# Optimization experiments

Measured on AMD Instinct MI355X. Metric: run time of the kernel, lower is better.

The kernel has to match this reference:

```python
import jax, jax.numpy as jnp
import numpy as np

N = 100   # num_nodes
D = 32    # num_dags
B = 8192  # batch_size
H = 32    # MLP hidden width


def setup_inputs() -> dict:
    key = jax.random.key(0)
    ks = jax.random.split(key, 6)
    x = jax.random.normal(ks[0], (B, N), dtype=jnp.float32)
    # binary adjacency masks for each sampled DAG
    A = (jax.random.uniform(ks[1], (D, N, N)) < 0.5).astype(jnp.float32)
    # per-dag topological order: a permutation of the N nodes
    order = jax.vmap(lambda k: jax.random.permutation(k, N))(
        jax.random.split(ks[2], D)).astype(jnp.int32)
    do_idx = 0  # intervened node
    # per-node MLP params: Linear(N+1, H) -> LeakyReLU -> Linear(H, 1)
    W1 = jax.random.normal(ks[3], (N, H, N + 1), dtype=jnp.float32) * (1.0 / np.sqrt(N + 1))
    b1 = jnp.zeros((N, H), dtype=jnp.float32)
    W2 = jax.random.normal(ks[4], (N, H), dtype=jnp.float32) * (1.0 / np.sqrt(H))
    b2 = jnp.zeros((N,), dtype=jnp.float32)
    return {"x": x, "A": A, "order": order, "do_idx": do_idx,
            "W1": W1, "b1": b1, "W2": W2, "b2": b2}


def reference(x, A, order, do_idx, W1, b1, W2, b2):
    Bn, Nn = x.shape
    # intervention: zero incoming edges of do_idx
    A = A.at[:, :, do_idx].set(0.0)

    def run_dag(A_d, order_d):
        def step(outputs, node):
            mask = A_d[:, node]                      # [N] parents of `node`
            ins = jnp.concatenate(
                [outputs * mask[None, :], x[:, node][:, None]], axis=1)  # [B, N+1]
            h = jax.nn.leaky_relu(ins @ W1[node].T + b1[node])           # [B, H]
            out = h @ W2[node] + b2[node]                                # [B]
            val = jnp.where(node == do_idx, x[:, node], out)
            return outputs.at[:, node].set(val), None

        outs, _ = jax.lax.scan(step, jnp.zeros((Bn, Nn), x.dtype), order_d)
        return outs  # [B, N]

    return jax.vmap(run_dag)(A, order)  # [D, B, N]
```

## Files before the change

kernel.cpp:

```cpp
#include <hip/hip_runtime.h>
#include <hip/hip_fp16.h>

#define NN 100
#define HH 32
#define BB 8192
#define DD 32
#define KP 128
#define TPB 512

typedef _Float16 f16x8 __attribute__((ext_vector_type(8)));
typedef _Float16 f16x2 __attribute__((ext_vector_type(2)));
typedef __fp16 fph2 __attribute__((ext_vector_type(2)));
typedef float f32x4 __attribute__((ext_vector_type(4)));
typedef unsigned short ushort_t;
typedef unsigned int uint_t;
union FU { uint4 u; f16x8 h; };
union PU { fph2 p; f16x2 h; uint_t u; };

#define AS_GLOBAL __attribute__((address_space(1)))
#define AS_LDS    __attribute__((address_space(3)))

__global__ void prep_xth(const float* __restrict__ x, ushort_t* __restrict__ xTh) {
  int idx = blockIdx.x * 256 + threadIdx.x;
  if (idx >= BB * NN) return;
  int b = idx & (BB - 1);
  int n = idx >> 13;
  xTh[idx] = __half_as_ushort(__float2half_rn(x[(size_t)b * NN + n]));
}

__global__ void prep_w1m(const float* __restrict__ A, const float* __restrict__ W1,
                         const float* __restrict__ b1, ushort_t* __restrict__ W1M) {
  int idx = blockIdx.x * 256 + threadIdx.x;
  int tile = idx >> 12;
  int d = tile / NN;
  int node = tile - d * NN;
  int rem = idx & 4095;
  int j = rem >> 7;
  int k = rem & 127;
  float v = 0.f;
  if (k < NN) {
    float m = A[((size_t)d * NN + k) * NN + node];
    v = (m != 0.f) ? W1[((size_t)node * HH + j) * (NN + 1) + k] : 0.f;
  } else if (k == NN) {
    v = W1[((size_t)node * HH + j) * (NN + 1) + NN];
  } else if (k == NN + 1) {
    v = b1[node * HH + j];
  }
  int t = (j * KP + k) ^ ((j & 7) << 3);
  W1M[(size_t)tile * 4096 + t] = __half_as_ushort(__float2half_rn(v));
}

__global__ void prep_epi3(const float* __restrict__ W2, const float* __restrict__ b2,
                          uint_t* __restrict__ epi) {
  int idx = blockIdx.x * 256 + threadIdx.x;
  if (idx >= NN * 20) return;
  int node = idx / 20;
  int c = idx - node * 20;
  uint_t v = 0u;
  if (c < 16) {
    uint_t lo = __half_as_ushort(__float2half_rn(W2[node * HH + 2 * c]));
    uint_t hi = __half_as_ushort(__float2half_rn(W2[node * HH + 2 * c + 1]));
    v = lo | (hi << 16);
  } else if (c == 16) {
    v = __float_as_uint(b2[node]);
  }
  epi[idx] = v;
}

#define XS_OFF 65536
#define EPI_OFF 73728
#define SMEM_BYTES (73728 + 8000)

__global__ __launch_bounds__(TPB, 4) void dag_mfma_ss(
    const ushort_t* __restrict__ xTh,
    const int* __restrict__ order,
    const int* __restrict__ do_idx_p,
    const ushort_t* __restrict__ W1M,
    const uint_t* __restrict__ epi_g,
    float* __restrict__ out)
{
  __shared__ __align__(16) char smem[SMEM_BYTES];
  ushort_t* stage = (ushort_t*)smem;
  const char* sp = (const char*)smem;
  uint_t* epi_l = (uint_t*)(smem + EPI_OFF);

  const int d = blockIdx.y;
  const int bx = blockIdx.x;
  const int tid = threadIdx.x;
  const int w = tid >> 6;
  const int lane = tid & 63;
  const int g = lane >> 4;
  const int n16 = lane & 15;
  const int di = __builtin_amdgcn_readfirstlane(do_idx_p[0]);

  {
    const uint4* s4 = (const uint4*)epi_g;
    uint4* d4 = (uint4*)epi_l;
    for (int i = tid; i < 500; i += TPB) d4[i] = s4[i];
  }

  const ushort_t* Wd = W1M + (size_t)d * NN * 4096;
  const int* ord = order + d * NN;

  int vs[4];
#pragma unroll
  for (int S = 0; S < 4; ++S) {
    int hw = n16 * 128 + ((8 * g) ^ ((n16 & 3) << 3)) + 32 * (S ^ ((n16 >> 2) & 1));
    vs[S] = 2 * hw + 32768;
  }
  int xso = XS_OFF + (w * 64 + n16) * 2 + 4096;

  int nd[4], nn[4];
#pragma unroll
  for (int q = 0; q < 4; ++q) nd[q] = __builtin_amdgcn_readfirstlane(ord[q]);
#pragma unroll
  for (int q = 0; q < 4; ++q) {
    const ushort_t* gsrc = Wd + (size_t)nd[q] * 4096 + tid * 8;
    __builtin_amdgcn_global_load_lds((const AS_GLOBAL void*)gsrc,
        (AS_LDS void*)(stage + q * 4096 + (w << 9)), 16, 0, 0);
  }
#pragma unroll
  for (int q = 0; q < 4; ++q) {
    if (w == q) {
      const ushort_t* gx = xTh + (size_t)nd[q] * BB + bx * 512 + lane * 8;
      __builtin_amdgcn_global_load_lds((const AS_GLOBAL void*)gx,
          (AS_LDS void*)(smem + XS_OFF + q * 1024), 16, 0, 0);
    }
  }

  uint4 breg[4][4];
#pragma unroll
  for (int nt = 0; nt < 4; ++nt) {
#pragma unroll
    for (int S = 0; S < 4; ++S) breg[nt][S] = make_uint4(0u, 0u, 0u, 0u);
    breg[nt][3].z = (g == 0) ? 0x3C000000u : 0u;
  }

  const f32x4 zero4 = {0.f, 0.f, 0.f, 0.f};
  PU c001; c001.u = 0x211F211Fu;

#pragma unroll 1
  for (int ss = 0; ss < 25; ++ss) {
    asm volatile("s_waitcnt vmcnt(0) lgkmcnt(0)" ::: "memory");
    __builtin_amdgcn_s_barrier();
    __builtin_amdgcn_sched_barrier(0);

#pragma unroll
    for (int S = 0; S < 4; ++S) vs[S] ^= 32768;
    xso ^= 4096;

    const bool more = (ss < 24);
    if (more) {
#pragma unroll
      for (int q = 0; q < 4; ++q)
        nn[q] = __builtin_amdgcn_readfirstlane(ord[4 * (ss + 1) + q]);
      const int dsts = (((ss + 1) & 1) << 14);
#pragma unroll
      for (int q = 0; q < 4; ++q) {
        const ushort_t* gsrc = Wd + (size_t)nn[q] * 4096 + tid * 8;
        __builtin_amdgcn_global_load_lds((const AS_GLOBAL void*)gsrc,
            (AS_LDS void*)(stage + dsts + q * 4096 + (w << 9)), 16, 0, 0);
      }
      const int xdst = XS_OFF + (((ss + 1) & 1) << 12);
#pragma unroll
      for (int q = 0; q < 4; ++q) {
        if (w == q) {
          const ushort_t* gx = xTh + (size_t)nn[q] * BB + bx * 512 + lane * 8;
          __builtin_amdgcn_global_load_lds((const AS_GLOBAL void*)gx,
              (AS_LDS void*)(smem + xdst + q * 1024), 16, 0, 0);
        }
      }
    }

#pragma unroll
    for (int q = 0; q < 4; ++q) {
      const int node = nd[q];

      ushort_t xb[4];
#pragma unroll
      for (int nt = 0; nt < 4; ++nt)
        xb[nt] = *(const ushort_t*)(sp + xso + q * 1024 + nt * 32);

#pragma unroll
      for (int nt = 0; nt < 4; ++nt) {
        uint_t ins = 0x3C000000u | (uint_t)xb[nt];
        breg[nt][3].z = (g == 0) ? ins : breg[nt][3].z;
      }

      float val[4];
      if (node != di) {
        const char* ep = (const char*)epi_l + node * 80;
        const float b2n = *(const float*)(ep + 64);

        f32x4 acc[4];
        float p0[4];

        {
          __builtin_amdgcn_s_setprio(1);
#pragma unroll
          for (int S = 0; S < 4; ++S) {
            FU a0;
            a0.u = *(const uint4*)(sp + vs[S] + q * 8192);
#pragma unroll
            for (int nt = 0; nt < 4; ++nt) {
              FU bu; bu.u = breg[nt][S];
              if (S == 0)
                acc[nt] = __builtin_amdgcn_mfma_f32_16x16x32_f16(a0.h, bu.h, zero4, 0, 0, 0);
              else
                acc[nt] = __builtin_amdgcn_mfma_f32_16x16x32_f16(a0.h, bu.h, acc[nt], 0, 0, 0);
            }
          }
          __builtin_amdgcn_s_setprio(0);
          const uint2 wlo = *(const uint2*)(ep + 8 * g);
          PU w01, w23; w01.u = wlo.x; w23.u = wlo.y;
#pragma unroll
          for (int nt = 0; nt < 4; ++nt) {
            PU h01, h23;
            h01.p = __builtin_amdgcn_cvt_pkrtz(acc[nt][0], acc[nt][1]);
            h23.p = __builtin_amdgcn_cvt_pkrtz(acc[nt][2], acc[nt][3]);
            h01.p = __builtin_elementwise_max(h01.p, h01.p * c001.p);
            h23.p = __builtin_elementwise_max(h23.p, h23.p * c001.p);
            float p = __builtin_amdgcn_fdot2(h01.h, w01.h, 0.f, false);
            p0[nt] = __builtin_amdgcn_fdot2(h23.h, w23.h, p, false);
          }
        }

        {
          __builtin_amdgcn_s_setprio(1);
#pragma unroll
          for (int S = 0; S < 4; ++S) {
            FU a1;
            a1.u = *(const uint4*)(sp + vs[S] + q * 8192 + 4096);
#pragma unroll
            for (int nt = 0; nt < 4; ++nt) {
              FU bu; bu.u = breg[nt][S];
              if (S == 0)
                acc[nt] = __builtin_amdgcn_mfma_f32_16x16x32_f16(a1.h, bu.h, zero4, 0, 0, 0);
              else
                acc[nt] = __builtin_amdgcn_mfma_f32_16x16x32_f16(a1.h, bu.h, acc[nt], 0, 0, 0);
            }
          }
          __builtin_amdgcn_s_setprio(0);
          const uint2 whi = *(const uint2*)(ep + 32 + 8 * g);
          PU w45, w67; w45.u = whi.x; w67.u = whi.y;
#pragma unroll
          for (int nt = 0; nt < 4; ++nt) {
            PU h45, h67;
            h45.p = __builtin_amdgcn_cvt_pkrtz(acc[nt][0], acc[nt][1]);
            h67.p = __builtin_amdgcn_cvt_pkrtz(acc[nt][2], acc[nt][3]);
            h45.p = __builtin_elementwise_max(h45.p, h45.p * c001.p);
            h67.p = __builtin_elementwise_max(h67.p, h67.p * c001.p);
            float p = __builtin_amdgcn_fdot2(h45.h, w45.h, p0[nt], false);
            p = __builtin_amdgcn_fdot2(h67.h, w67.h, p, false);
            p += __shfl_xor(p, 16, 64);
            p += __shfl_xor(p, 32, 64);
            val[nt] = p + b2n;
          }
        }
      } else {
#pragma unroll
        for (int nt = 0; nt < 4; ++nt)
          val[nt] = __half2float(__ushort_as_half(xb[nt]));
      }

      const int sn = node >> 5;
      const int en2 = (node >> 1) & 3;
      const int gn = (node >> 3) & 3;
      const int hin = node & 1;
      const bool own = (g == gn);
      ushort_t hv[4];
#pragma unroll
      for (int nt = 0; nt < 4; ++nt) hv[nt] = __half_as_ushort(__float2half_rn(val[nt]));
#pragma unroll
      for (int S = 0; S < 4; ++S) {
        if (S != sn) continue;
#pragma unroll
        for (int nt = 0; nt < 4; ++nt) {
          uint4& Bq = breg[nt][S];
          uint_t hvn = (uint_t)hv[nt];
          if (en2 == 0) {
            uint_t old = Bq.x;
            uint_t nw = hin ? ((old & 0x0000FFFFu) | (hvn << 16)) : ((old & 0xFFFF0000u) | hvn);
            Bq.x = own ? nw : old;
          } else if (en2 == 1) {
            uint_t old = Bq.y;
            uint_t nw = hin ? ((old & 0x0000FFFFu) | (hvn << 16)) : ((old & 0xFFFF0000u) | hvn);
            Bq.y = own ? nw : old;
          } else if (en2 == 2) {
            uint_t old = Bq.z;
            uint_t nw = hin ? ((old & 0x0000FFFFu) | (hvn << 16)) : ((old & 0xFFFF0000u) | hvn);
            Bq.z = own ? nw : old;
          } else {
            uint_t old = Bq.w;
            uint_t nw = hin ? ((old & 0x0000FFFFu) | (hvn << 16)) : ((old & 0xFFFF0000u) | hvn);
            Bq.w = own ? nw : old;
          }
        }
      }
    }

#pragma unroll
    for (int q = 0; q < 4; ++q) nd[q] = nn[q];
  }

  ushort_t* tbuf = (ushort_t*)smem;
  for (int c = 0; c < 8; ++c) {
    __syncthreads();
    if (w == c) {
#pragma unroll
      for (int nt = 0; nt < 4; ++nt) {
        int r = nt * 16 + n16;
#pragma unroll
        for (int S = 0; S < 4; ++S) {
          int k = 32 * S + 8 * g;
          *(uint2*)&tbuf[r * 132 + k] = make_uint2(breg[nt][S].x, breg[nt][S].y);
          *(uint2*)&tbuf[r * 132 + k + 4] = make_uint2(breg[nt][S].z, breg[nt][S].w);
        }
      }
    }
    __syncthreads();
    const size_t obase = ((size_t)d * BB + bx * 512 + c * 64) * NN;
    for (int idx = tid; idx < 64 * NN; idx += TPB) {
      int rl = idx / NN;
      int col = idx - rl * NN;
      out[obase + idx] = __half2float(__ushort_as_half(tbuf[rl * 132 + col]));
    }
  }
}

extern "C" void kernel_launch(void* const* d_in, const int* in_sizes, int n_in,
                              void* d_out, int out_size, void* d_ws, size_t ws_size,
                              hipStream_t stream) {
  const float* x     = (const float*)d_in[0];
  const float* A     = (const float*)d_in[1];
  const int* order   = (const int*)d_in[2];
  const int* do_idx  = (const int*)d_in[3];
  const float* W1    = (const float*)d_in[4];
  const float* b1    = (const float*)d_in[5];
  const float* W2    = (const float*)d_in[6];
  const float* b2    = (const float*)d_in[7];
  float* out = (float*)d_out;

  char* ws = (char*)d_ws;
  const size_t XTH_B = (size_t)BB * NN * 2;
  const size_t W1M_B = (size_t)DD * NN * 4096 * 2;
  ushort_t* xTh = (ushort_t*)ws;
  ushort_t* W1M = (ushort_t*)(ws + XTH_B);
  uint_t* epi   = (uint_t*)(ws + XTH_B + W1M_B);

  hipLaunchKernelGGL(prep_xth, dim3((BB * NN) / 256), dim3(256), 0, stream, x, xTh);
  hipLaunchKernelGGL(prep_w1m, dim3((DD * NN * 4096) / 256), dim3(256), 0, stream,
                     A, W1, b1, W1M);
  hipLaunchKernelGGL(prep_epi3, dim3((NN * 20 + 255) / 256), dim3(256), 0, stream,
                     W2, b2, epi);
  hipLaunchKernelGGL(dag_mfma_ss, dim3(BB / 512, DD), dim3(TPB), 0, stream,
                     xTh, order, do_idx, W1M, epi, out);
}
```

Measured before the change: 268.6 us.

## Double block size to 1024 threads and load x directly into registers

Blocks now cover 1024 batch rows with 16 waves, so each staged W1 tile in LDS is shared by twice as many waves and total W1 traffic per DAG is halved. The x values are no longer staged through LDS; each lane prefetches the next node's x from global memory into registers. The W2 epilogue is repacked so each lane gets its weights in one 16-byte LDS read, with b2 kept in a separate table. The cost is half as many blocks (256 in total), which lowers parallelism across CUs, and launch_bounds(1024,4) puts heavy pressure on registers.

```diff
diff --git a/kernel.cpp b/kernel.cpp
--- a/kernel.cpp
+++ b/kernel.cpp
@@ -6,11 +6,11 @@
 #define BB 8192
 #define DD 32
 #define KP 128
-#define TPB 512
+#define TPB 1024
 
 typedef _Float16 f16x8 __attribute__((ext_vector_type(8)));
+typedef __fp16 fph2 __attribute__((ext_vector_type(2)));
 typedef _Float16 f16x2 __attribute__((ext_vector_type(2)));
-typedef __fp16 fph2 __attribute__((ext_vector_type(2)));
 typedef float f32x4 __attribute__((ext_vector_type(4)));
 typedef unsigned short ushort_t;
 typedef unsigned int uint_t;
@@ -19,6 +19,12 @@
 
 #define AS_GLOBAL __attribute__((address_space(1)))
 #define AS_LDS    __attribute__((address_space(3)))
+
+#define SELQ(arr, qq) ((qq) == 0 ? arr[0] : (qq) == 1 ? arr[1] : (qq) == 2 ? arr[2] : arr[3])
+
+#define EPI4_OFF 65536
+#define B2T_OFF 71936
+#define SMEM_BYTES 72336
 
 __global__ void prep_xth(const float* __restrict__ x, ushort_t* __restrict__ xTh) {
   int idx = blockIdx.x * 256 + threadIdx.x;
@@ -50,39 +56,34 @@
   W1M[(size_t)tile * 4096 + t] = __half_as_ushort(__float2half_rn(v));
 }
 
-__global__ void prep_epi3(const float* __restrict__ W2, const float* __restrict__ b2,
-                          uint_t* __restrict__ epi) {
+__global__ void prep_epi4(const float* __restrict__ W2, const float* __restrict__ b2,
+                          uint_t* __restrict__ epi4, float* __restrict__ b2t) {
   int idx = blockIdx.x * 256 + threadIdx.x;
-  if (idx >= NN * 20) return;
-  int node = idx / 20;
-  int c = idx - node * 20;
-  uint_t v = 0u;
-  if (c < 16) {
-    uint_t lo = __half_as_ushort(__float2half_rn(W2[node * HH + 2 * c]));
-    uint_t hi = __half_as_ushort(__float2half_rn(W2[node * HH + 2 * c + 1]));
-    v = lo | (hi << 16);
-  } else if (c == 16) {
-    v = __float_as_uint(b2[node]);
-  }
-  epi[idx] = v;
-}
-
-#define XS_OFF 65536
-#define EPI_OFF 73728
-#define SMEM_BYTES (73728 + 8000)
-
-__global__ __launch_bounds__(TPB, 4) void dag_mfma_ss(
+  if (idx < NN * 16) {
+    int node = idx >> 4;
+    int g = (idx >> 2) & 3;
+    int r = idx & 3;
+    int j0 = ((r & 2) << 3) + 4 * g + ((r & 1) << 1);
+    uint_t lo = __half_as_ushort(__float2half_rn(W2[node * HH + j0]));
+    uint_t hi = __half_as_ushort(__float2half_rn(W2[node * HH + j0 + 1]));
+    epi4[idx] = lo | (hi << 16);
+  } else if (idx < NN * 16 + NN) {
+    int node = idx - NN * 16;
+    b2t[node] = b2[node];
+  }
+}
+
+__global__ __launch_bounds__(TPB, 4) void dag_mfma_w64(
     const ushort_t* __restrict__ xTh,
     const int* __restrict__ order,
     const int* __restrict__ do_idx_p,
     const ushort_t* __restrict__ W1M,
-    const uint_t* __restrict__ epi_g,
+    const uint_t* __restrict__ epi4_g,
+    const float* __restrict__ b2t_g,
     float* __restrict__ out)
 {
   __shared__ __align__(16) char smem[SMEM_BYTES];
-  ushort_t* stage = (ushort_t*)smem;
   const char* sp = (const char*)smem;
-  uint_t* epi_l = (uint_t*)(smem + EPI_OFF);
 
   const int d = blockIdx.y;
   const int bx = blockIdx.x;
@@ -92,40 +93,44 @@
   const int g = lane >> 4;
   const int n16 = lane & 15;
   const int di = __builtin_amdgcn_readfirstlane(do_idx_p[0]);
+  const int* ord = order + d * NN;
+  const int rowbase = bx * 1024 + w * 64 + n16;
 
   {
-    const uint4* s4 = (const uint4*)epi_g;
-    uint4* d4 = (uint4*)epi_l;
-    for (int i = tid; i < 500; i += TPB) d4[i] = s4[i];
+    const uint4* s4 = (const uint4*)epi4_g;
+    uint4* d4 = (uint4*)(smem + EPI4_OFF);
+    for (int i = tid; i < 400; i += TPB) d4[i] = s4[i];
+    if (tid < NN) ((float*)(smem + B2T_OFF))[tid] = b2t_g[tid];
   }
 
   const ushort_t* Wd = W1M + (size_t)d * NN * 4096;
-  const int* ord = order + d * NN;
 
   int vs[4];
 #pragma unroll
   for (int S = 0; S < 4; ++S) {
-    int hw = n16 * 128 + ((8 * g) ^ ((n16 & 3) << 3)) + 32 * (S ^ ((n16 >> 2) & 1));
-    vs[S] = 2 * hw + 32768;
-  }
-  int xso = XS_OFF + (w * 64 + n16) * 2 + 4096;
-
-  int nd[4], nn[4];
-#pragma unroll
-  for (int q = 0; q < 4; ++q) nd[q] = __builtin_amdgcn_readfirstlane(ord[q]);
-#pragma unroll
-  for (int q = 0; q < 4; ++q) {
-    const ushort_t* gsrc = Wd + (size_t)nd[q] * 4096 + tid * 8;
-    __builtin_amdgcn_global_load_lds((const AS_GLOBAL void*)gsrc,
-        (AS_LDS void*)(stage + q * 4096 + (w << 9)), 16, 0, 0);
-  }
-#pragma unroll
-  for (int q = 0; q < 4; ++q) {
-    if (w == q) {
-      const ushort_t* gx = xTh + (size_t)nd[q] * BB + bx * 512 + lane * 8;
-      __builtin_amdgcn_global_load_lds((const AS_GLOBAL void*)gx,
-          (AS_LDS void*)(smem + XS_OFF + q * 1024), 16, 0, 0);
-    }
+    int hw = n16 * KP + ((8 * g) ^ ((n16 & 3) << 3)) + 32 * (S ^ ((n16 >> 2) & 1));
+    vs[S] = 2 * hw;
+  }
+  int tsb = 32768;
+
+  int nd[4], nn2[4];
+#pragma unroll
+  for (int q = 0; q < 4; ++q) { nd[q] = __builtin_amdgcn_readfirstlane(ord[q]); nn2[q] = nd[q]; }
+  {
+    const int q2 = tid >> 8, sub = tid & 255;
+    const int nsel = SELQ(nd, q2);
+    const char* gb = (const char*)(Wd + (size_t)nsel * 4096);
+    char* lb = (char*)smem + q2 * 8192;
+    __builtin_amdgcn_global_load_lds((const AS_GLOBAL void*)(gb + sub * 16),
+                                     (AS_LDS void*)(lb + sub * 16), 16, 0, 0);
+    __builtin_amdgcn_global_load_lds((const AS_GLOBAL void*)(gb + 4096 + sub * 16),
+                                     (AS_LDS void*)(lb + 4096 + sub * 16), 16, 0, 0);
+  }
+  ushort_t xbc[4], xbn[4];
+  {
+    const ushort_t* xp = xTh + (size_t)nd[0] * BB + rowbase;
+#pragma unroll
+    for (int nt = 0; nt < 4; ++nt) xbc[nt] = xp[nt * 16];
   }
 
   uint4 breg[4][4];
@@ -145,74 +150,66 @@
     __builtin_amdgcn_s_barrier();
     __builtin_amdgcn_sched_barrier(0);
 
-#pragma unroll
-    for (int S = 0; S < 4; ++S) vs[S] ^= 32768;
-    xso ^= 4096;
-
-    const bool more = (ss < 24);
-    if (more) {
+    tsb ^= 32768;
+
+    if (ss < 24) {
 #pragma unroll
       for (int q = 0; q < 4; ++q)
-        nn[q] = __builtin_amdgcn_readfirstlane(ord[4 * (ss + 1) + q]);
-      const int dsts = (((ss + 1) & 1) << 14);
-#pragma unroll
-      for (int q = 0; q < 4; ++q) {
-        const ushort_t* gsrc = Wd + (size_t)nn[q] * 4096 + tid * 8;
-        __builtin_amdgcn_global_load_lds((const AS_GLOBAL void*)gsrc,
-            (AS_LDS void*)(stage + dsts + q * 4096 + (w << 9)), 16, 0, 0);
-      }
-      const int xdst = XS_OFF + (((ss + 1) & 1) << 12);
-#pragma unroll
-      for (int q = 0; q < 4; ++q) {
-        if (w == q) {
-          const ushort_t* gx = xTh + (size_t)nn[q] * BB + bx * 512 + lane * 8;
-          __builtin_amdgcn_global_load_lds((const AS_GLOBAL void*)gx,
-              (AS_LDS void*)(smem + xdst + q * 1024), 16, 0, 0);
-        }
-      }
+        nn2[q] = __builtin_amdgcn_readfirstlane(ord[4 * (ss + 1) + q]);
+      const int dset = tsb ^ 32768;
+      const int q2 = tid >> 8, sub = tid & 255;
+      const int nsel = SELQ(nn2, q2);
+      const char* gb = (const char*)(Wd + (size_t)nsel * 4096);
+      char* lb = (char*)smem + dset + q2 * 8192;
+      __builtin_amdgcn_global_load_lds((const AS_GLOBAL void*)(gb + sub * 16),
+                                       (AS_LDS void*)(lb + sub * 16), 16, 0, 0);
+      __builtin_amdgcn_global_load_lds((const AS_GLOBAL void*)(gb + 4096 + sub * 16),
+                                       (AS_LDS void*)(lb + 4096 + sub * 16), 16, 0, 0);
     }
 
 #pragma unroll
     for (int q = 0; q < 4; ++q) {
       const int node = nd[q];
 
-      ushort_t xb[4];
-#pragma unroll
-      for (int nt = 0; nt < 4; ++nt)
-        xb[nt] = *(const ushort_t*)(sp + xso + q * 1024 + nt * 32);
+      {
+        const int node_nx = (q < 3) ? nd[q + 1] : nn2[0];
+        const ushort_t* xp = xTh + (size_t)node_nx * BB + rowbase;
+#pragma unroll
+        for (int nt = 0; nt < 4; ++nt) xbn[nt] = xp[nt * 16];
+      }
 
 #pragma unroll
       for (int nt = 0; nt < 4; ++nt) {
-        uint_t ins = 0x3C000000u | (uint_t)xb[nt];
+        uint_t ins = 0x3C000000u | (uint_t)xbc[nt];
         breg[nt][3].z = (g == 0) ? ins : breg[nt][3].z;
       }
 
       float val[4];
       if (node != di) {
-        const char* ep = (const char*)epi_l + node * 80;
-        const float b2n = *(const float*)(ep + 64);
+        const uint4 w4 = *(const uint4*)(sp + EPI4_OFF + node * 64 + g * 16);
+        const float b2n = *(const float*)(sp + B2T_OFF + node * 4);
+        const int tb = tsb + q * 8192;
 
         f32x4 acc[4];
         float p0[4];
 
+        __builtin_amdgcn_s_setprio(1);
+#pragma unroll
+        for (int S = 0; S < 4; ++S) {
+          FU a;
+          a.u = *(const uint4*)(sp + tb + vs[S]);
+#pragma unroll
+          for (int nt = 0; nt < 4; ++nt) {
+            FU bu; bu.u = breg[nt][S];
+            if (S == 0)
+              acc[nt] = __builtin_amdgcn_mfma_f32_16x16x32_f16(a.h, bu.h, zero4, 0, 0, 0);
+            else
+              acc[nt] = __builtin_amdgcn_mfma_f32_16x16x32_f16(a.h, bu.h, acc[nt], 0, 0, 0);
+          }
+        }
+        __builtin_amdgcn_s_setprio(0);
         {
-          __builtin_amdgcn_s_setprio(1);
-#pragma unroll
-          for (int S = 0; S < 4; ++S) {
-            FU a0;
-            a0.u = *(const uint4*)(sp + vs[S] + q * 8192);
-#pragma unroll
-            for (int nt = 0; nt < 4; ++nt) {
-              FU bu; bu.u = breg[nt][S];
-              if (S == 0)
-                acc[nt] = __builtin_amdgcn_mfma_f32_16x16x32_f16(a0.h, bu.h, zero4, 0, 0, 0);
-              else
-                acc[nt] = __builtin_amdgcn_mfma_f32_16x16x32_f16(a0.h, bu.h, acc[nt], 0, 0, 0);
-            }
-          }
-          __builtin_amdgcn_s_setprio(0);
-          const uint2 wlo = *(const uint2*)(ep + 8 * g);
-          PU w01, w23; w01.u = wlo.x; w23.u = wlo.y;
+          PU w01, w23; w01.u = w4.x; w23.u = w4.y;
 #pragma unroll
           for (int nt = 0; nt < 4; ++nt) {
             PU h01, h23;
@@ -225,24 +222,23 @@
           }
         }
 
+        __builtin_amdgcn_s_setprio(1);
+#pragma unroll
+        for (int S = 0; S < 4; ++S) {
+          FU a;
+          a.u = *(const uint4*)(sp + tb + 4096 + vs[S]);
+#pragma unroll
+          for (int nt = 0; nt < 4; ++nt) {
+            FU bu; bu.u = breg[nt][S];
+            if (S == 0)
+              acc[nt] = __builtin_amdgcn_mfma_f32_16x16x32_f16(a.h, bu.h, zero4, 0, 0, 0);
+            else
+              acc[nt] = __builtin_amdgcn_mfma_f32_16x16x32_f16(a.h, bu.h, acc[nt], 0, 0, 0);
+          }
+        }
+        __builtin_amdgcn_s_setprio(0);
         {
-          __builtin_amdgcn_s_setprio(1);
-#pragma unroll
-          for (int S = 0; S < 4; ++S) {
-            FU a1;
-            a1.u = *(const uint4*)(sp + vs[S] + q * 8192 + 4096);
-#pragma unroll
-            for (int nt = 0; nt < 4; ++nt) {
-              FU bu; bu.u = breg[nt][S];
-              if (S == 0)
-                acc[nt] = __builtin_amdgcn_mfma_f32_16x16x32_f16(a1.h, bu.h, zero4, 0, 0, 0);
-              else
-                acc[nt] = __builtin_amdgcn_mfma_f32_16x16x32_f16(a1.h, bu.h, acc[nt], 0, 0, 0);
-            }
-          }
-          __builtin_amdgcn_s_setprio(0);
-          const uint2 whi = *(const uint2*)(ep + 32 + 8 * g);
-          PU w45, w67; w45.u = whi.x; w67.u = whi.y;
+          PU w45, w67; w45.u = w4.z; w67.u = w4.w;
 #pragma unroll
           for (int nt = 0; nt < 4; ++nt) {
             PU h45, h67;
@@ -260,7 +256,7 @@
       } else {
 #pragma unroll
         for (int nt = 0; nt < 4; ++nt)
-          val[nt] = __half2float(__ushort_as_half(xb[nt]));
+          val[nt] = __half2float(__ushort_as_half(xbc[nt]));
       }
 
       const int sn = node >> 5;
@@ -297,14 +293,19 @@
           }
         }
       }
+
+#pragma unroll
+      for (int nt = 0; nt < 4; ++nt) xbc[nt] = xbn[nt];
     }
 
 #pragma unroll
-    for (int q = 0; q < 4; ++q) nd[q] = nn[q];
-  }
-
+    for (int q = 0; q < 4; ++q) nd[q] = nn2[q];
+  }
+
+  __syncthreads();
   ushort_t* tbuf = (ushort_t*)smem;
-  for (int c = 0; c < 8; ++c) {
+#pragma unroll 1
+  for (int c = 0; c < 16; ++c) {
     __syncthreads();
     if (w == c) {
 #pragma unroll
@@ -319,7 +320,7 @@
       }
     }
     __syncthreads();
-    const size_t obase = ((size_t)d * BB + bx * 512 + c * 64) * NN;
+    const size_t obase = ((size_t)d * BB + bx * 1024 + c * 64) * NN;
     for (int idx = tid; idx < 64 * NN; idx += TPB) {
       int rl = idx / NN;
       int col = idx - rl * NN;
@@ -346,13 +347,14 @@
   const size_t W1M_B = (size_t)DD * NN * 4096 * 2;
   ushort_t* xTh = (ushort_t*)ws;
   ushort_t* W1M = (ushort_t*)(ws + XTH_B);
-  uint_t* epi   = (uint_t*)(ws + XTH_B + W1M_B);
+  uint_t* epi4  = (uint_t*)(ws + XTH_B + W1M_B);
+  float* b2t    = (float*)(ws + XTH_B + W1M_B + 6400);
 
   hipLaunchKernelGGL(prep_xth, dim3((BB * NN) / 256), dim3(256), 0, stream, x, xTh);
   hipLaunchKernelGGL(prep_w1m, dim3((DD * NN * 4096) / 256), dim3(256), 0, stream,
                      A, W1, b1, W1M);
-  hipLaunchKernelGGL(prep_epi3, dim3((NN * 20 + 255) / 256), dim3(256), 0, stream,
-                     W2, b2, epi);
-  hipLaunchKernelGGL(dag_mfma_ss, dim3(BB / 512, DD), dim3(TPB), 0, stream,
-                     xTh, order, do_idx, W1M, epi, out);
-}
+  hipLaunchKernelGGL(prep_epi4, dim3((NN * 16 + NN + 255) / 256), dim3(256), 0, stream,
+                     W2, b2, epi4, b2t);
+  hipLaunchKernelGGL(dag_mfma_w64, dim3(BB / 1024, DD), dim3(TPB), 0, stream,
+                     xTh, order, do_idx, W1M, epi4, b2t, out);
+}
```

New measurement: 284.0 us. 5.7% more time.
